# Kernel tuning notes

Measured on AMD Instinct MI355X. Metric: run time of the kernel, lower is better.

## Reference

```python
import jax, jax.numpy as jnp
import numpy as np

N_UP, N_DOWN = 8, 8
N_ELEC = N_UP + N_DOWN
N_NUC = 4
D, K, F, H = 128, 64, 32, 45  # embedding, kernel, dist_feat, w-MLP hidden (log-spaced)
CUTOFF = 10.0
B = 2048


def _pairs(a, b):
    s, r = np.meshgrid(a, b, indexing='ij')
    return s.ravel(), r.ravel()


def _edges():
    up = np.arange(N_UP)
    dn = np.arange(N_UP, N_ELEC)
    su, ru = _pairs(up, up); m = su != ru; su, ru = su[m], ru[m]
    sd, rd = _pairs(dn, dn); m = sd != rd; sd, rd = sd[m], rd[m]
    same_s = np.concatenate([su, sd]); same_r = np.concatenate([ru, rd])
    a1s, a1r = _pairs(up, dn); a2s, a2r = _pairs(dn, up)
    anti_s = np.concatenate([a1s, a2s]); anti_r = np.concatenate([a1r, a2r])
    ne_s = np.repeat(np.arange(N_NUC), N_ELEC)
    ne_r = np.tile(np.arange(N_ELEC), N_NUC)
    return tuple(jnp.asarray(x, jnp.int32) for x in (same_s, same_r, anti_s, anti_r, ne_s, ne_r))


def setup_inputs() -> dict:
    key = jax.random.key(0)
    ks = jax.random.split(key, 10)
    rs = jax.random.normal(ks[0], (B, N_ELEC, 3)) * 2.0
    coords = jax.random.normal(ks[1], (N_NUC, 3)) * 2.0
    X_tab = jax.random.normal(ks[2], (1, D))
    Y_w = jax.random.normal(ks[3], (N_NUC, K)) / np.sqrt(N_NUC)
    wW1 = jax.random.normal(ks[4], (3, 3, F, H)) / np.sqrt(F)
    wb1 = jax.random.normal(ks[5], (3, 3, H)) * 0.1
    wW2 = jax.random.normal(ks[6], (3, 3, H, K)) / np.sqrt(H)
    h0_tab = jax.random.normal(ks[7], (2, 1, K))
    hW = jax.random.normal(ks[8], (2, 2, D, K)) / np.sqrt(D)
    gW = jax.random.normal(ks[9], (3, 3, K, D)) / np.sqrt(K)
    same_s, same_r, anti_s, anti_r, ne_s, ne_r = _edges()
    return dict(rs=rs, coords=coords, X_tab=X_tab, Y_w=Y_w, wW1=wW1, wb1=wb1,
                wW2=wW2, h0_tab=h0_tab, hW=hW, gW=gW,
                same_s=same_s, same_r=same_r, anti_s=anti_s, anti_r=anti_r,
                ne_s=ne_s, ne_r=ne_r)


def _dist_basis(d):
    # DistanceBasis with 'nocusp' envelope: env = d^2 exp(-d), gaussians at mus
    qs = jnp.linspace(0.0, 1.0, F)
    mus = CUTOFF * qs ** 2
    sigmas = (1.0 + CUTOFF * qs) / 7.0
    env = d ** 2 * jnp.exp(-d)
    return env[..., None] * jnp.exp(-((d[..., None] - mus) ** 2) / sigmas ** 2)


def reference(rs, coords, X_tab, Y_w, wW1, wb1, wW2, h0_tab, hW, gW,
              same_s, same_r, anti_s, anti_r, ne_s, ne_r):
    Bn = rs.shape[0]
    spin_idxs = jnp.zeros((N_ELEC,), jnp.int32)  # n_up == n_down -> one spin class
    # per-edge distances (layer-0 update_edges_fn featurizes them once)
    d_same = jnp.linalg.norm(rs[:, same_s] - rs[:, same_r], axis=-1)  # [B,112]
    d_anti = jnp.linalg.norm(rs[:, anti_s] - rs[:, anti_r], axis=-1)  # [B,128]
    d_ne = jnp.linalg.norm(coords[ne_s][None] - rs[:, ne_r], axis=-1)  # [B,64]
    feats = [_dist_basis(d_same), _dist_basis(d_anti), _dist_basis(d_ne)]
    senders = [same_s, anti_s, ne_s]
    receivers = [same_r, anti_r, ne_r]
    elec = X_tab[spin_idxs]  # [N_ELEC, D] electron embedding X(spin_idxs)
    nuc = Y_w                # Y(eye(n_nuc)) == Y_w, [N_NUC, K]
    for l in range(3):
        upd = 0.0
        for j in range(3):  # same, anti, ne
            # w subnet: 2-layer MLP, silu hidden with bias, bias-free linear out
            we = jax.nn.silu(feats[j] @ wW1[l, j] + wb1[l, j]) @ wW2[l, j]  # [B,E,K]
            if j < 2:
                if l == 0:
                    hx = h0_tab[j][spin_idxs][senders[j]]            # [E,K] embed
                else:
                    hx = (elec @ hW[l - 1, j])[:, senders[j]]        # [B,E,K]
                weh = we * hx
            else:
                weh = we * nuc[ne_s][None]                           # [B,E,K]
            # segment_sum scatter into receiver electrons
            z = jnp.zeros((Bn, N_ELEC, K), we.dtype).at[:, receivers[j]].add(weh)
            upd = upd + z @ gW[l, j]                                  # [B,N_ELEC,D]
        elec = elec + upd
    return elec
```

## Files before the change

### kernel.cpp

```cpp
#include <hip/hip_runtime.h>
#include <hip/hip_bf16.h>

#define NE 16
#define NN 4
#define DDIM 128
#define KD 64
#define HD 45

typedef _Float16 half8 __attribute__((ext_vector_type(8)));
typedef float floatx4 __attribute__((ext_vector_type(4)));

#define OFF_FLAG_B 0
#define OFF_B1_B   64
#define OFF_XT_B   1792
#define OFF_H0_B   2304
#define OFF_YW_B   2560
#define OFF_W1_B   3072
#define OFF_W2_B   30720
#define OFF_GW_B   104448
#define OFF_HW_B   251904
#define OFF_RL_B   317440

__device__ __forceinline__ float ldf(const void* p, long i, int f32) {
    if (f32) return ((const float*)p)[i];
    unsigned int u = ((unsigned int)((const unsigned short*)p)[i]) << 16;
    return __uint_as_float(u);
}

__global__ void detect_kernel(const unsigned short* rs16, char* wsB) {
    __shared__ int bad;
    if (threadIdx.x == 0) bad = 0;
    __syncthreads();
    for (int i = threadIdx.x; i < 2048; i += 256) {
        unsigned int u = ((unsigned int)rs16[i]) << 16;
        float v = __uint_as_float(u);
        if (!(fabsf(v) < 1e6f)) atomicOr(&bad, 1);
    }
    __syncthreads();
    if (threadIdx.x == 0) *(int*)(wsB + OFF_FLAG_B) = bad ? 1 : 0;
}

__global__ void prep_kernel(const void* w1, const void* b1, const void* w2, const void* h0,
                            const void* hW, const void* gW, const void* Yw, const void* Xt,
                            char* wsB) {
    const int f32 = *(const int*)(wsB + OFF_FLAG_B);
    int i = blockIdx.x * 256 + threadIdx.x;
    _Float16* W1F = (_Float16*)(wsB + OFF_W1_B);
    _Float16* W2F = (_Float16*)(wsB + OFF_W2_B);
    _Float16* GWF = (_Float16*)(wsB + OFF_GW_B);
    _Float16* HWF = (_Float16*)(wsB + OFF_HW_B);
    float*    B1  = (float*)(wsB + OFF_B1_B);
    float*    XT  = (float*)(wsB + OFF_XT_B);
    _Float16* H0F = (_Float16*)(wsB + OFF_H0_B);
    _Float16* YWF = (_Float16*)(wsB + OFF_YW_B);

    if (i < 13824) {
        int lj = i / 1536, rem = i % 1536;
        int nt = rem >> 9, lane = (rem & 511) >> 3, e = rem & 7;
        int row = ((lane >> 4) << 3) + e;
        int col = (nt << 4) + (lane & 15);
        W1F[i] = (_Float16)((col < 45) ? ldf(w1, lj * 1440 + row * 45 + col, f32) : 0.f);
    }
    if (i < 36864) {
        int lj = i / 4096, rem = i & 4095;
        int nt = rem >> 10, kt = (rem >> 9) & 1, lane = (rem & 511) >> 3, e = rem & 7;
        int row = (kt << 5) + ((lane >> 4) << 3) + e;
        int col = (nt << 4) + (lane & 15);
        W2F[i] = (_Float16)((row < 45) ? ldf(w2, lj * 2880 + row * 64 + col, f32) : 0.f);
    }
    if (i < 73728) {
        int lj = i >> 13, rem = i & 8191;
        int nt = rem >> 10, kt = (rem >> 9) & 1, lane = (rem & 511) >> 3, e = rem & 7;
        int row = (kt << 5) + ((lane >> 4) << 3) + e;
        int col = (nt << 4) + (lane & 15);
        GWF[i] = (_Float16)ldf(gW, lj * 8192 + row * 128 + col, f32);
    }
    if (i < 32768) {
        int lj = i >> 13, rem = i & 8191;
        int nt = rem >> 11, kt = (rem >> 9) & 3, lane = (rem & 511) >> 3, e = rem & 7;
        int row = (kt << 5) + ((lane >> 4) << 3) + e;
        int col = (nt << 4) + (lane & 15);
        HWF[i] = (_Float16)ldf(hW, lj * 8192 + row * 64 + col, f32);
    }
    if (i < 432) { int lj = i / 48, n = i % 48; B1[i] = (n < 45) ? ldf(b1, lj * 45 + n, f32) : 0.f; }
    if (i < 128) XT[i] = ldf(Xt, i, f32);
    if (i < 128) H0F[i] = (_Float16)ldf(h0, i, f32);
    if (i < 256) YWF[i] = (_Float16)ldf(Yw, i, f32);
}

__global__ void rlbuild_kernel(const int* __restrict__ same_s, const int* __restrict__ same_r,
                               const int* __restrict__ anti_s, const int* __restrict__ anti_r,
                               const int* __restrict__ ne_s,   const int* __restrict__ ne_r,
                               char* wsB) {
    int lane = threadIdx.x;
    if (lane >= 48) return;
    int j = lane >> 4, r = lane & 15;
    int* rl = (int*)(wsB + OFF_RL_B) + lane * 8;
    int cnt  = (j == 0) ? 112 : ((j == 1) ? 128 : 64);
    const int* rr = (j == 0) ? same_r : ((j == 1) ? anti_r : ne_r);
    const int* ss = (j == 0) ? same_s : ((j == 1) ? anti_s : ne_s);
    int n = 0;
    for (int i = 0; i < cnt && n < 8; ++i)
        if (rr[i] == r) { rl[n++] = i | (ss[i] << 16); }
    for (; n < 8; ++n) rl[n] = 0;
}

__device__ __forceinline__ half8 feat_tile(
    const void* __restrict__ rs, const void* __restrict__ coords,
    int b, int lm, int f32, int tloc, int cls,
    const int* __restrict__ S, const int* __restrict__ R,
    const float* __restrict__ A0, const float* __restrict__ B0, const float* __restrict__ C0)
{
    int le = tloc * 16 + lm;
    int s = S[le], r = R[le];
    long rb = ((long)b * NE + r) * 3;
    float bx = ldf(rs, rb + 0, f32), by = ldf(rs, rb + 1, f32), bz = ldf(rs, rb + 2, f32);
    float ax, ay, az;
    if (cls < 2) {
        long sb = ((long)b * NE + s) * 3;
        ax = ldf(rs, sb + 0, f32); ay = ldf(rs, sb + 1, f32); az = ldf(rs, sb + 2, f32);
    } else {
        ax = ldf(coords, s * 3 + 0, f32); ay = ldf(coords, s * 3 + 1, f32); az = ldf(coords, s * 3 + 2, f32);
    }
    float dx = ax - bx, dy = ay - by, dz = az - bz;
    float d = sqrtf(dx * dx + dy * dy + dz * dz);
    float d2 = d * d;
    half8 a;
    #pragma unroll
    for (int ii = 0; ii < 8; ++ii) {
        float E = fmaf(A0[ii], d2, fmaf(B0[ii], d, C0[ii]));
        a[ii] = (_Float16)(d2 * __expf(E));
    }
    return a;
}

__device__ __forceinline__ void we_tile(
    half8 fa, int lj, int tt,
    const char* __restrict__ wsB, _Float16* __restrict__ hid,
    _Float16* __restrict__ weS, int lane, int qd, int lm)
{
    const half8* W1F_lj = (const half8*)(wsB + OFF_W1_B) + lj * 192;
    half8 w0 = W1F_lj[lane], w1v = W1F_lj[64 + lane], w2v = W1F_lj[128 + lane];
    const float* B1 = (const float*)(wsB + OFF_B1_B) + lj * 48;
    float bi0 = B1[lm], bi1 = B1[16 + lm], bi2 = B1[32 + lm];
    floatx4 c0 = {0.f,0.f,0.f,0.f}, c1 = c0, c2 = c0;
    c0 = __builtin_amdgcn_mfma_f32_16x16x32_f16(fa, w0,  c0, 0, 0, 0);
    c1 = __builtin_amdgcn_mfma_f32_16x16x32_f16(fa, w1v, c1, 0, 0, 0);
    c2 = __builtin_amdgcn_mfma_f32_16x16x32_f16(fa, w2v, c2, 0, 0, 0);
    #pragma unroll
    for (int rr = 0; rr < 4; ++rr) {
        int row = qd * 4 + rr;
        float v0 = c0[rr] + bi0, v1 = c1[rr] + bi1, v2 = c2[rr] + bi2;
        v0 = v0 * __builtin_amdgcn_rcpf(1.f + __expf(-v0));
        v1 = v1 * __builtin_amdgcn_rcpf(1.f + __expf(-v1));
        v2 = v2 * __builtin_amdgcn_rcpf(1.f + __expf(-v2));
        hid[row * 64 + lm]      = (_Float16)v0;
        hid[row * 64 + 16 + lm] = (_Float16)v1;
        hid[row * 64 + 32 + lm] = (_Float16)v2;
    }
    half8 a0 = *(const half8*)(hid + lm * 64 + qd * 8);
    half8 a1 = *(const half8*)(hid + lm * 64 + 32 + qd * 8);
    const half8* W2F_lj = (const half8*)(wsB + OFF_W2_B) + lj * 512;
    _Float16* wrow = weS + tt * 1024;
    #pragma unroll
    for (int nt = 0; nt < 4; ++nt) {
        half8 bk0 = W2F_lj[nt * 128 + lane], bk1 = W2F_lj[nt * 128 + 64 + lane];
        floatx4 acc = {0.f,0.f,0.f,0.f};
        acc = __builtin_amdgcn_mfma_f32_16x16x32_f16(a0, bk0, acc, 0, 0, 0);
        acc = __builtin_amdgcn_mfma_f32_16x16x32_f16(a1, bk1, acc, 0, 0, 0);
        #pragma unroll
        for (int rr = 0; rr < 4; ++rr)
            wrow[(qd * 4 + rr) * 64 + nt * 16 + lm] = (_Float16)acc[rr];
    }
}

template<int J, int CNT>
__device__ __forceinline__ void scatter_zf_gmm(
    int L, int wv, int lane, int qd, int lm,
    const _Float16* __restrict__ weS, const _Float16* __restrict__ hxrow,
    const int* __restrict__ rlS, float* __restrict__ zS,
    const half8* __restrict__ GWF, floatx4 (&eacc)[2])
{
    #pragma unroll
    for (int rr4 = 0; rr4 < 4; ++rr4) {
        const int r = wv * 4 + rr4;
        const int* rlj = rlS + (J * 16 + r) * 8;
        float acc = 0.f;
        #pragma unroll
        for (int i = 0; i < CNT; ++i) {
            int pk = rlj[i];
            int e = pk & 0xFFFF, s = pk >> 16;
            acc += (float)weS[e * 64 + lane] * (float)hxrow[s * 64 + lane];
        }
        zS[r * 68 + lane] = acc;
    }
    __syncthreads();
    half8 zf0, zf1;
    {
        const float* zr = zS + lm * 68 + qd * 8;
        floatx4 va = *(const floatx4*)zr;
        floatx4 vb = *(const floatx4*)(zr + 4);
        floatx4 vc = *(const floatx4*)(zr + 32);
        floatx4 vd = *(const floatx4*)(zr + 36);
        #pragma unroll
        for (int ii = 0; ii < 4; ++ii) {
            zf0[ii] = (_Float16)va[ii]; zf0[4 + ii] = (_Float16)vb[ii];
            zf1[ii] = (_Float16)vc[ii]; zf1[4 + ii] = (_Float16)vd[ii];
        }
    }
    const half8* G = GWF + (size_t)(L * 3 + J) * 1024;
    #pragma unroll
    for (int u = 0; u < 2; ++u) {
        int t2 = wv * 2 + u;
        eacc[u] = __builtin_amdgcn_mfma_f32_16x16x32_f16(zf0, G[t2 * 128 + lane],      eacc[u], 0, 0, 0);
        eacc[u] = __builtin_amdgcn_mfma_f32_16x16x32_f16(zf1, G[t2 * 128 + 64 + lane], eacc[u], 0, 0, 0);
    }
    __syncthreads();
}

__global__ __launch_bounds__(256, 4)
void fused_kernel(const void* __restrict__ rs, const void* __restrict__ coords,
                  const int* __restrict__ same_s, const int* __restrict__ same_r,
                  const int* __restrict__ anti_s, const int* __restrict__ anti_r,
                  const int* __restrict__ ne_s,   const int* __restrict__ ne_r,
                  const char* __restrict__ wsB, void* __restrict__ out)
{
    const int b = blockIdx.x;
    const int tid = threadIdx.x;
    const int wv = tid >> 6, lane = tid & 63;
    const int qd = lane >> 4, lm = lane & 15;
    const int f32 = *(const int*)(wsB + OFF_FLAG_B);

    __shared__ __align__(16) _Float16 weS[128 * 64];
    __shared__ __align__(16) _Float16 hidA[4][1024];
    __shared__ float zS[16 * 68];
    __shared__ _Float16 hxS[2 * 1024];
    __shared__ _Float16 nucS[256];
    __shared__ __align__(16) _Float16 elecB[16 * 136];
    __shared__ int rlS[384];

    const _Float16* H0F = (const _Float16*)(wsB + OFF_H0_B);
    const _Float16* YWF = (const _Float16*)(wsB + OFF_YW_B);
    const float*    XT  = (const float*)(wsB + OFF_XT_B);
    const half8*    GWF = (const half8*)(wsB + OFF_GW_B);
    const half8*    HWF = (const half8*)(wsB + OFF_HW_B);

    for (int i = tid; i < 384; i += 256) rlS[i] = ((const int*)(wsB + OFF_RL_B))[i];
    for (int i = tid; i < 2048; i += 256) hxS[i] = H0F[((i >> 10) << 6) + (i & 63)];
    if (tid < 256) nucS[tid] = YWF[tid];

    _Float16* hid = hidA[wv];
    {
        half8 z8 = {0,0,0,0,0,0,0,0};
        *(half8*)(hid + lane * 8) = z8;
        *(half8*)(hid + 512 + lane * 8) = z8;
    }

    float A0[8], B0[8], C0[8];
    #pragma unroll
    for (int ii = 0; ii < 8; ++ii) {
        float qf = (float)(qd * 8 + ii) * (1.f / 31.f);
        float mu = 10.f * qf * qf;
        float u = 7.f * __builtin_amdgcn_rcpf(1.f + 10.f * qf);
        float is2 = u * u;
        A0[ii] = -is2;
        B0[ii] = 2.f * mu * is2 - 1.f;
        C0[ii] = -(mu * mu) * is2;
    }

    half8 fa_s0 = feat_tile(rs, coords, b, lm, f32, wv,     0, same_s, same_r, A0, B0, C0);
    half8 fa_s1 = {0,0,0,0,0,0,0,0};
    if (wv < 3)
          fa_s1 = feat_tile(rs, coords, b, lm, f32, wv + 4, 0, same_s, same_r, A0, B0, C0);
    half8 fa_a0 = feat_tile(rs, coords, b, lm, f32, wv,     1, anti_s, anti_r, A0, B0, C0);
    half8 fa_a1 = feat_tile(rs, coords, b, lm, f32, wv + 4, 1, anti_s, anti_r, A0, B0, C0);
    half8 fa_n  = feat_tile(rs, coords, b, lm, f32, wv,     2, ne_s,   ne_r,   A0, B0, C0);

    floatx4 eacc[2];
    #pragma unroll
    for (int u = 0; u < 2; ++u) {
        float xv = XT[(wv * 2 + u) * 16 + lm];
        eacc[u][0] = xv; eacc[u][1] = xv; eacc[u][2] = xv; eacc[u][3] = xv;
    }
    __syncthreads();

    for (int L = 0; L < 3; ++L) {
        const int lj0 = L * 3;
        we_tile(fa_s0, lj0 + 0, wv, wsB, hid, weS, lane, qd, lm);
        if (wv < 3) we_tile(fa_s1, lj0 + 0, wv + 4, wsB, hid, weS, lane, qd, lm);
        __syncthreads();
        scatter_zf_gmm<0, 7>(L, wv, lane, qd, lm, weS, hxS, rlS, zS, GWF, eacc);
        we_tile(fa_a0, lj0 + 1, wv,     wsB, hid, weS, lane, qd, lm);
        we_tile(fa_a1, lj0 + 1, wv + 4, wsB, hid, weS, lane, qd, lm);
        __syncthreads();
        scatter_zf_gmm<1, 8>(L, wv, lane, qd, lm, weS, hxS + 1024, rlS, zS, GWF, eacc);
        we_tile(fa_n, lj0 + 2, wv, wsB, hid, weS, lane, qd, lm);
        __syncthreads();
        scatter_zf_gmm<2, 4>(L, wv, lane, qd, lm, weS, nucS, rlS, zS, GWF, eacc);

        if (L < 2) {
            #pragma unroll
            for (int u = 0; u < 2; ++u) {
                int t2 = wv * 2 + u;
                #pragma unroll
                for (int r = 0; r < 4; ++r)
                    elecB[(qd * 4 + r) * 136 + t2 * 16 + lm] = (_Float16)eacc[u][r];
            }
            __syncthreads();
            half8 ae[4];
            #pragma unroll
            for (int kt = 0; kt < 4; ++kt)
                ae[kt] = *(const half8*)(elecB + lm * 136 + kt * 32 + qd * 8);
            #pragma unroll
            for (int u = 0; u < 2; ++u) {
                int idx = wv * 2 + u;
                int j = idx >> 2, nt = idx & 3;
                floatx4 acc = {0.f,0.f,0.f,0.f};
                #pragma unroll
                for (int kt = 0; kt < 4; ++kt) {
                    half8 g = HWF[(size_t)(((L * 2 + j) * 4 + nt) * 4 + kt) * 64 + lane];
                    acc = __builtin_amdgcn_mfma_f32_16x16x32_f16(ae[kt], g, acc, 0, 0, 0);
                }
                #pragma unroll
                for (int r = 0; r < 4; ++r)
                    hxS[j * 1024 + (qd * 4 + r) * 64 + nt * 16 + lm] = (_Float16)acc[r];
            }
        }
    }

    if (f32) {
        float* o = (float*)out + (size_t)b * 2048;
        #pragma unroll
        for (int u = 0; u < 2; ++u)
            #pragma unroll
            for (int r = 0; r < 4; ++r)
                o[(qd * 4 + r) * 128 + (wv * 2 + u) * 16 + lm] = eacc[u][r];
    } else {
        __hip_bfloat16* o = (__hip_bfloat16*)out + (size_t)b * 2048;
        #pragma unroll
        for (int u = 0; u < 2; ++u)
            #pragma unroll
            for (int r = 0; r < 4; ++r)
                o[(qd * 4 + r) * 128 + (wv * 2 + u) * 16 + lm] = __float2bfloat16(eacc[u][r]);
    }
}

extern "C" void kernel_launch(void* const* d_in, const int* in_sizes, int n_in,
                              void* d_out, int out_size, void* d_ws, size_t ws_size,
                              hipStream_t stream) {
    const void* rs     = d_in[0];
    const void* coords = d_in[1];
    const void* X_tab  = d_in[2];
    const void* Y_w    = d_in[3];
    const void* wW1    = d_in[4];
    const void* wb1    = d_in[5];
    const void* wW2    = d_in[6];
    const void* h0     = d_in[7];
    const void* hW     = d_in[8];
    const void* gW     = d_in[9];
    const int* same_s = (const int*)d_in[10];
    const int* same_r = (const int*)d_in[11];
    const int* anti_s = (const int*)d_in[12];
    const int* anti_r = (const int*)d_in[13];
    const int* ne_s   = (const int*)d_in[14];
    const int* ne_r   = (const int*)d_in[15];
    char* wsB = (char*)d_ws;

    const int Bn = in_sizes[0] / (NE * 3);

    detect_kernel<<<1, 256, 0, stream>>>((const unsigned short*)rs, wsB);
    prep_kernel<<<288, 256, 0, stream>>>(wW1, wb1, wW2, h0, hW, gW, Y_w, X_tab, wsB);
    rlbuild_kernel<<<1, 64, 0, stream>>>(same_s, same_r, anti_s, anti_r, ne_s, ne_r, wsB);
    fused_kernel<<<Bn, 256, 0, stream>>>(rs, coords, same_s, same_r, anti_s, anti_r,
                                         ne_s, ne_r, wsB, d_out);
}
```

Before: 225.7 us.

## Replace scalar scatter with indicator-matrix MFMA and merge prep kernels

```diff
diff --git a/kernel.cpp b/kernel.cpp
--- a/kernel.cpp
+++ b/kernel.cpp
@@ -8,6 +8,7 @@
 #define HD 45
 
 typedef _Float16 half8 __attribute__((ext_vector_type(8)));
+typedef _Float16 half4 __attribute__((ext_vector_type(4)));
 typedef float floatx4 __attribute__((ext_vector_type(4)));
 
 #define OFF_FLAG_B 0
@@ -19,7 +20,6 @@
 #define OFF_W2_B   30720
 #define OFF_GW_B   104448
 #define OFF_HW_B   251904
-#define OFF_RL_B   317440
 
 __device__ __forceinline__ float ldf(const void* p, long i, int f32) {
     if (f32) return ((const float*)p)[i];
@@ -27,23 +27,26 @@
     return __uint_as_float(u);
 }
 
-__global__ void detect_kernel(const unsigned short* rs16, char* wsB) {
-    __shared__ int bad;
-    if (threadIdx.x == 0) bad = 0;
+__global__ void prep2_kernel(const void* w1, const void* b1, const void* w2, const void* h0,
+                             const void* hW, const void* gW, const void* Yw, const void* Xt,
+                             const void* rs, char* wsB) {
+    __shared__ int badS;
+    if (threadIdx.x == 0) badS = 0;
     __syncthreads();
-    for (int i = threadIdx.x; i < 2048; i += 256) {
-        unsigned int u = ((unsigned int)rs16[i]) << 16;
-        float v = __uint_as_float(u);
-        if (!(fabsf(v) < 1e6f)) atomicOr(&bad, 1);
+    {
+        const unsigned short* rs16 = (const unsigned short*)rs;
+        int bad = 0;
+        for (int i = threadIdx.x; i < 2048; i += 256) {
+            unsigned int u = ((unsigned int)rs16[i]) << 16;
+            float v = __uint_as_float(u);
+            if (!(fabsf(v) < 1e6f)) bad = 1;
+        }
+        if (bad) atomicOr(&badS, 1);
     }
     __syncthreads();
-    if (threadIdx.x == 0) *(int*)(wsB + OFF_FLAG_B) = bad ? 1 : 0;
-}
-
-__global__ void prep_kernel(const void* w1, const void* b1, const void* w2, const void* h0,
-                            const void* hW, const void* gW, const void* Yw, const void* Xt,
-                            char* wsB) {
-    const int f32 = *(const int*)(wsB + OFF_FLAG_B);
+    const int f32 = badS ? 1 : 0;
+    if (blockIdx.x == 0 && threadIdx.x == 0) *(int*)(wsB + OFF_FLAG_B) = f32;
+
     int i = blockIdx.x * 256 + threadIdx.x;
     _Float16* W1F = (_Float16*)(wsB + OFF_W1_B);
     _Float16* W2F = (_Float16*)(wsB + OFF_W2_B);
@@ -86,23 +89,6 @@
     if (i < 128) XT[i] = ldf(Xt, i, f32);
     if (i < 128) H0F[i] = (_Float16)ldf(h0, i, f32);
     if (i < 256) YWF[i] = (_Float16)ldf(Yw, i, f32);
-}
-
-__global__ void rlbuild_kernel(const int* __restrict__ same_s, const int* __restrict__ same_r,
-                               const int* __restrict__ anti_s, const int* __restrict__ anti_r,
-                               const int* __restrict__ ne_s,   const int* __restrict__ ne_r,
-                               char* wsB) {
-    int lane = threadIdx.x;
-    if (lane >= 48) return;
-    int j = lane >> 4, r = lane & 15;
-    int* rl = (int*)(wsB + OFF_RL_B) + lane * 8;
-    int cnt  = (j == 0) ? 112 : ((j == 1) ? 128 : 64);
-    const int* rr = (j == 0) ? same_r : ((j == 1) ? anti_r : ne_r);
-    const int* ss = (j == 0) ? same_s : ((j == 1) ? anti_s : ne_s);
-    int n = 0;
-    for (int i = 0; i < cnt && n < 8; ++i)
-        if (rr[i] == r) { rl[n++] = i | (ss[i] << 16); }
-    for (; n < 8; ++n) rl[n] = 0;
 }
 
 __device__ __forceinline__ half8 feat_tile(
@@ -134,10 +120,13 @@
     return a;
 }
 
-__device__ __forceinline__ void we_tile(
-    half8 fa, int lj, int tt,
+__device__ __forceinline__ void we_tile_weh(
+    half8 fa, int lj, int tile,
     const char* __restrict__ wsB, _Float16* __restrict__ hid,
-    _Float16* __restrict__ weS, int lane, int qd, int lm)
+    const _Float16* __restrict__ hxrow,
+    const unsigned char* __restrict__ sendC,
+    _Float16* __restrict__ wehT,
+    int lane, int qd, int lm)
 {
     const half8* W1F_lj = (const half8*)(wsB + OFF_W1_B) + lj * 192;
     half8 w0 = W1F_lj[lane], w1v = W1F_lj[64 + lane], w2v = W1F_lj[128 + lane];
@@ -150,72 +139,71 @@
     #pragma unroll
     for (int rr = 0; rr < 4; ++rr) {
         int row = qd * 4 + rr;
+        int x = (row & 7) << 4;
         float v0 = c0[rr] + bi0, v1 = c1[rr] + bi1, v2 = c2[rr] + bi2;
         v0 = v0 * __builtin_amdgcn_rcpf(1.f + __expf(-v0));
         v1 = v1 * __builtin_amdgcn_rcpf(1.f + __expf(-v1));
         v2 = v2 * __builtin_amdgcn_rcpf(1.f + __expf(-v2));
-        hid[row * 64 + lm]      = (_Float16)v0;
-        hid[row * 64 + 16 + lm] = (_Float16)v1;
-        hid[row * 64 + 32 + lm] = (_Float16)v2;
-    }
-    half8 a0 = *(const half8*)(hid + lm * 64 + qd * 8);
-    half8 a1 = *(const half8*)(hid + lm * 64 + 32 + qd * 8);
+        char* hb = (char*)hid + row * 128;
+        *(_Float16*)(hb + ((lm * 2)      ^ x)) = (_Float16)v0;
+        *(_Float16*)(hb + ((32 + lm * 2) ^ x)) = (_Float16)v1;
+        *(_Float16*)(hb + ((64 + lm * 2) ^ x)) = (_Float16)v2;
+    }
+    int xr = (lm & 7) << 4;
+    half8 a0 = *(const half8*)((const char*)hid + lm * 128 + ((qd * 16)      ^ xr));
+    half8 a1 = *(const half8*)((const char*)hid + lm * 128 + ((64 + qd * 16) ^ xr));
+
+    int sv0 = sendC[tile * 16 + qd * 4 + 0];
+    int sv1 = sendC[tile * 16 + qd * 4 + 1];
+    int sv2 = sendC[tile * 16 + qd * 4 + 2];
+    int sv3 = sendC[tile * 16 + qd * 4 + 3];
+
     const half8* W2F_lj = (const half8*)(wsB + OFF_W2_B) + lj * 512;
-    _Float16* wrow = weS + tt * 1024;
     #pragma unroll
     for (int nt = 0; nt < 4; ++nt) {
         half8 bk0 = W2F_lj[nt * 128 + lane], bk1 = W2F_lj[nt * 128 + 64 + lane];
         floatx4 acc = {0.f,0.f,0.f,0.f};
         acc = __builtin_amdgcn_mfma_f32_16x16x32_f16(a0, bk0, acc, 0, 0, 0);
         acc = __builtin_amdgcn_mfma_f32_16x16x32_f16(a1, bk1, acc, 0, 0, 0);
-        #pragma unroll
-        for (int rr = 0; rr < 4; ++rr)
-            wrow[(qd * 4 + rr) * 64 + nt * 16 + lm] = (_Float16)acc[rr];
-    }
-}
-
-template<int J, int CNT>
-__device__ __forceinline__ void scatter_zf_gmm(
-    int L, int wv, int lane, int qd, int lm,
-    const _Float16* __restrict__ weS, const _Float16* __restrict__ hxrow,
-    const int* __restrict__ rlS, float* __restrict__ zS,
-    const half8* __restrict__ GWF, floatx4 (&eacc)[2])
-{
-    #pragma unroll
-    for (int rr4 = 0; rr4 < 4; ++rr4) {
-        const int r = wv * 4 + rr4;
-        const int* rlj = rlS + (J * 16 + r) * 8;
-        float acc = 0.f;
-        #pragma unroll
-        for (int i = 0; i < CNT; ++i) {
-            int pk = rlj[i];
-            int e = pk & 0xFFFF, s = pk >> 16;
-            acc += (float)weS[e * 64 + lane] * (float)hxrow[s * 64 + lane];
-        }
-        zS[r * 68 + lane] = acc;
-    }
-    __syncthreads();
-    half8 zf0, zf1;
-    {
-        const float* zr = zS + lm * 68 + qd * 8;
-        floatx4 va = *(const floatx4*)zr;
-        floatx4 vb = *(const floatx4*)(zr + 4);
-        floatx4 vc = *(const floatx4*)(zr + 32);
-        floatx4 vd = *(const floatx4*)(zr + 36);
-        #pragma unroll
-        for (int ii = 0; ii < 4; ++ii) {
-            zf0[ii] = (_Float16)va[ii]; zf0[4 + ii] = (_Float16)vb[ii];
-            zf1[ii] = (_Float16)vc[ii]; zf1[4 + ii] = (_Float16)vd[ii];
-        }
-    }
-    const half8* G = GWF + (size_t)(L * 3 + J) * 1024;
+        const int kc = nt * 16 + lm;
+        const int eb = tile * 16 + qd * 4;
+        wehT[kc * 136 + eb + 0] = (_Float16)(acc[0] * (float)hxrow[sv0 * 68 + kc]);
+        wehT[kc * 136 + eb + 1] = (_Float16)(acc[1] * (float)hxrow[sv1 * 68 + kc]);
+        wehT[kc * 136 + eb + 2] = (_Float16)(acc[2] * (float)hxrow[sv2 * 68 + kc]);
+        wehT[kc * 136 + eb + 3] = (_Float16)(acc[3] * (float)hxrow[sv3 * 68 + kc]);
+    }
+}
+
+template<int NC>
+__device__ __forceinline__ void z_mfma(
+    const _Float16* __restrict__ wehT, const half8* __restrict__ ind,
+    _Float16* __restrict__ zh, int wv, int qd, int lm)
+{
+    floatx4 zD = {0.f,0.f,0.f,0.f};
+    #pragma unroll
+    for (int c = 0; c < NC; ++c) {
+        half8 A = *(const half8*)(wehT + (wv * 16 + lm) * 136 + c * 32 + qd * 8);
+        zD = __builtin_amdgcn_mfma_f32_16x16x32_f16(A, ind[c], zD, 0, 0, 0);
+    }
+    half4 h;
+    #pragma unroll
+    for (int i = 0; i < 4; ++i) h[i] = (_Float16)zD[i];
+    *(half4*)(zh + lm * 72 + wv * 16 + qd * 4) = h;
+}
+
+__device__ __forceinline__ void gw_accum(
+    int L, int j, int wv, int lane, int qd, int lm,
+    const _Float16* __restrict__ zh, const half8* __restrict__ GWF, floatx4 (&eacc)[2])
+{
+    half8 zf0 = *(const half8*)(zh + lm * 72 + qd * 8);
+    half8 zf1 = *(const half8*)(zh + lm * 72 + 32 + qd * 8);
+    const half8* G = GWF + (size_t)(L * 3 + j) * 1024;
     #pragma unroll
     for (int u = 0; u < 2; ++u) {
         int t2 = wv * 2 + u;
         eacc[u] = __builtin_amdgcn_mfma_f32_16x16x32_f16(zf0, G[t2 * 128 + lane],      eacc[u], 0, 0, 0);
         eacc[u] = __builtin_amdgcn_mfma_f32_16x16x32_f16(zf1, G[t2 * 128 + 64 + lane], eacc[u], 0, 0, 0);
     }
-    __syncthreads();
 }
 
 __global__ __launch_bounds__(256, 4)
@@ -231,13 +219,13 @@
     const int qd = lane >> 4, lm = lane & 15;
     const int f32 = *(const int*)(wsB + OFF_FLAG_B);
 
-    __shared__ __align__(16) _Float16 weS[128 * 64];
+    __shared__ __align__(16) _Float16 wehT[64 * 136];
     __shared__ __align__(16) _Float16 hidA[4][1024];
-    __shared__ float zS[16 * 68];
-    __shared__ _Float16 hxS[2 * 1024];
-    __shared__ _Float16 nucS[256];
+    __shared__ __align__(16) _Float16 zhS[16 * 72];
+    __shared__ _Float16 hxS[2 * 1088];
+    __shared__ _Float16 nucS[4 * 68];
     __shared__ __align__(16) _Float16 elecB[16 * 136];
-    __shared__ int rlS[384];
+    __shared__ unsigned char sendPad[384], recvPad[384];
 
     const _Float16* H0F = (const _Float16*)(wsB + OFF_H0_B);
     const _Float16* YWF = (const _Float16*)(wsB + OFF_YW_B);
@@ -245,36 +233,61 @@
     const half8*    GWF = (const half8*)(wsB + OFF_GW_B);
     const half8*    HWF = (const half8*)(wsB + OFF_HW_B);
 
-    for (int i = tid; i < 384; i += 256) rlS[i] = ((const int*)(wsB + OFF_RL_B))[i];
-    for (int i = tid; i < 2048; i += 256) hxS[i] = H0F[((i >> 10) << 6) + (i & 63)];
-    if (tid < 256) nucS[tid] = YWF[tid];
-
-    _Float16* hid = hidA[wv];
+    for (int i = tid; i < 384; i += 256) {
+        int cls = i >> 7, pos = i & 127;
+        int cnt = (cls == 0) ? 112 : ((cls == 1) ? 128 : 64);
+        int s = 0, r = 255;
+        if (pos < cnt) {
+            if (cls == 0)      { s = same_s[pos]; r = same_r[pos]; }
+            else if (cls == 1) { s = anti_s[pos]; r = anti_r[pos]; }
+            else               { s = ne_s[pos];   r = ne_r[pos]; }
+        }
+        sendPad[i] = (unsigned char)s; recvPad[i] = (unsigned char)r;
+    }
+    for (int i = tid; i < 2048; i += 256)
+        hxS[(i >> 10) * 1088 + ((i >> 6) & 15) * 68 + (i & 63)] = H0F[((i >> 10) << 6) + (i & 63)];
+    if (tid < 256) nucS[(tid >> 6) * 68 + (tid & 63)] = YWF[tid];
+    for (int i = tid; i < 4352; i += 256) ((unsigned int*)wehT)[i] = 0u;
     {
+        _Float16* hid = hidA[wv];
         half8 z8 = {0,0,0,0,0,0,0,0};
         *(half8*)(hid + lane * 8) = z8;
         *(half8*)(hid + 512 + lane * 8) = z8;
     }
-
-    float A0[8], B0[8], C0[8];
-    #pragma unroll
-    for (int ii = 0; ii < 8; ++ii) {
-        float qf = (float)(qd * 8 + ii) * (1.f / 31.f);
-        float mu = 10.f * qf * qf;
-        float u = 7.f * __builtin_amdgcn_rcpf(1.f + 10.f * qf);
-        float is2 = u * u;
-        A0[ii] = -is2;
-        B0[ii] = 2.f * mu * is2 - 1.f;
-        C0[ii] = -(mu * mu) * is2;
-    }
-
-    half8 fa_s0 = feat_tile(rs, coords, b, lm, f32, wv,     0, same_s, same_r, A0, B0, C0);
-    half8 fa_s1 = {0,0,0,0,0,0,0,0};
-    if (wv < 3)
-          fa_s1 = feat_tile(rs, coords, b, lm, f32, wv + 4, 0, same_s, same_r, A0, B0, C0);
-    half8 fa_a0 = feat_tile(rs, coords, b, lm, f32, wv,     1, anti_s, anti_r, A0, B0, C0);
-    half8 fa_a1 = feat_tile(rs, coords, b, lm, f32, wv + 4, 1, anti_s, anti_r, A0, B0, C0);
-    half8 fa_n  = feat_tile(rs, coords, b, lm, f32, wv,     2, ne_s,   ne_r,   A0, B0, C0);
+    __syncthreads();
+
+    half8 ind[10];
+    #pragma unroll
+    for (int c = 0; c < 10; ++c) {
+        const int cls = (c < 4) ? 0 : ((c < 8) ? 1 : 2);
+        const int lc  = c - ((cls == 0) ? 0 : ((cls == 1) ? 4 : 8));
+        #pragma unroll
+        for (int ii = 0; ii < 8; ++ii) {
+            int e = lc * 32 + qd * 8 + ii;
+            ind[c][ii] = (recvPad[cls * 128 + e] == lm) ? (_Float16)1.0f : (_Float16)0.0f;
+        }
+    }
+
+    half8 fa_s0, fa_s1 = {0,0,0,0,0,0,0,0}, fa_a0, fa_a1, fa_n;
+    {
+        float A0[8], B0[8], C0[8];
+        #pragma unroll
+        for (int ii = 0; ii < 8; ++ii) {
+            float qf = (float)(qd * 8 + ii) * (1.f / 31.f);
+            float mu = 10.f * qf * qf;
+            float u = 7.f * __builtin_amdgcn_rcpf(1.f + 10.f * qf);
+            float is2 = u * u;
+            A0[ii] = -is2;
+            B0[ii] = 2.f * mu * is2 - 1.f;
+            C0[ii] = -(mu * mu) * is2;
+        }
+        fa_s0 = feat_tile(rs, coords, b, lm, f32, wv,     0, same_s, same_r, A0, B0, C0);
+        if (wv < 3)
+        fa_s1 = feat_tile(rs, coords, b, lm, f32, wv + 4, 0, same_s, same_r, A0, B0, C0);
+        fa_a0 = feat_tile(rs, coords, b, lm, f32, wv,     1, anti_s, anti_r, A0, B0, C0);
+        fa_a1 = feat_tile(rs, coords, b, lm, f32, wv + 4, 1, anti_s, anti_r, A0, B0, C0);
+        fa_n  = feat_tile(rs, coords, b, lm, f32, wv,     2, ne_s,   ne_r,   A0, B0, C0);
+    }
 
     floatx4 eacc[2];
     #pragma unroll
@@ -282,21 +295,29 @@
         float xv = XT[(wv * 2 + u) * 16 + lm];
         eacc[u][0] = xv; eacc[u][1] = xv; eacc[u][2] = xv; eacc[u][3] = xv;
     }
-    __syncthreads();
+
+    _Float16* hid = hidA[wv];
 
     for (int L = 0; L < 3; ++L) {
         const int lj0 = L * 3;
-        we_tile(fa_s0, lj0 + 0, wv, wsB, hid, weS, lane, qd, lm);
-        if (wv < 3) we_tile(fa_s1, lj0 + 0, wv + 4, wsB, hid, weS, lane, qd, lm);
-        __syncthreads();
-        scatter_zf_gmm<0, 7>(L, wv, lane, qd, lm, weS, hxS, rlS, zS, GWF, eacc);
-        we_tile(fa_a0, lj0 + 1, wv,     wsB, hid, weS, lane, qd, lm);
-        we_tile(fa_a1, lj0 + 1, wv + 4, wsB, hid, weS, lane, qd, lm);
-        __syncthreads();
-        scatter_zf_gmm<1, 8>(L, wv, lane, qd, lm, weS, hxS + 1024, rlS, zS, GWF, eacc);
-        we_tile(fa_n, lj0 + 2, wv, wsB, hid, weS, lane, qd, lm);
-        __syncthreads();
-        scatter_zf_gmm<2, 4>(L, wv, lane, qd, lm, weS, nucS, rlS, zS, GWF, eacc);
+        we_tile_weh(fa_s0, lj0, wv, wsB, hid, hxS, sendPad, wehT, lane, qd, lm);
+        if (wv < 3)
+        we_tile_weh(fa_s1, lj0, wv + 4, wsB, hid, hxS, sendPad, wehT, lane, qd, lm);
+        __syncthreads();
+        z_mfma<4>(wehT, ind + 0, zhS, wv, qd, lm);
+        __syncthreads();
+        gw_accum(L, 0, wv, lane, qd, lm, zhS, GWF, eacc);
+        we_tile_weh(fa_a0, lj0 + 1, wv,     wsB, hid, hxS + 1088, sendPad + 128, wehT, lane, qd, lm);
+        we_tile_weh(fa_a1, lj0 + 1, wv + 4, wsB, hid, hxS + 1088, sendPad + 128, wehT, lane, qd, lm);
+        __syncthreads();
+        z_mfma<4>(wehT, ind + 4, zhS, wv, qd, lm);
+        __syncthreads();
+        gw_accum(L, 1, wv, lane, qd, lm, zhS, GWF, eacc);
+        we_tile_weh(fa_n, lj0 + 2, wv, wsB, hid, nucS, sendPad + 256, wehT, lane, qd, lm);
+        __syncthreads();
+        z_mfma<2>(wehT, ind + 8, zhS, wv, qd, lm);
+        __syncthreads();
+        gw_accum(L, 2, wv, lane, qd, lm, zhS, GWF, eacc);
 
         if (L < 2) {
             #pragma unroll
@@ -323,8 +344,9 @@
                 }
                 #pragma unroll
                 for (int r = 0; r < 4; ++r)
-                    hxS[j * 1024 + (qd * 4 + r) * 64 + nt * 16 + lm] = (_Float16)acc[r];
+                    hxS[j * 1088 + (qd * 4 + r) * 68 + nt * 16 + lm] = (_Float16)acc[r];
             }
+            __syncthreads();
         }
     }
 
@@ -368,9 +390,7 @@
 
     const int Bn = in_sizes[0] / (NE * 3);
 
-    detect_kernel<<<1, 256, 0, stream>>>((const unsigned short*)rs, wsB);
-    prep_kernel<<<288, 256, 0, stream>>>(wW1, wb1, wW2, h0, hW, gW, Y_w, X_tab, wsB);
-    rlbuild_kernel<<<1, 64, 0, stream>>>(same_s, same_r, anti_s, anti_r, ne_s, ne_r, wsB);
+    prep2_kernel<<<288, 256, 0, stream>>>(wW1, wb1, wW2, h0, hW, gW, Y_w, X_tab, rs, wsB);
     fused_kernel<<<Bn, 256, 0, stream>>>(rs, coords, same_s, same_r, anti_s, anti_r,
                                          ne_s, ne_r, wsB, d_out);
 }
```

New measurement: 227.1 us. Within noise of the previous version (+0.6%).
